# Performance work log

Hardware: AMD Instinct MI355X
Metric: run time of the kernel (lower is better)

Reference implementation:

```python
import jax, jax.numpy as jnp
import numpy as np


def _rms_norm(x, g, eps=1e-6):
    # WanRMSNorm over the full channel dim
    return x * jax.lax.rsqrt(jnp.mean(x * x, axis=-1, keepdims=True) + eps) * g


def _rope_apply(x, angles, f, h, w, start_frame):
    # x: [B, L, n, d]; angles: [1024, d//2] (real rotation angles; torch version
    # stores exp(i*theta) complex and multiplies in float64 -- same rotation math).
    B, L, n, d = x.shape
    c = d // 2
    c1 = c // 3
    c0 = c - 2 * c1  # band split [22, 21, 21] for c=64
    af = angles[start_frame:start_frame + f, :c0]        # [f, c0]
    ah = angles[:h, c0:c0 + c1]                          # [h, c1]
    aw = angles[:w, c0 + c1:]                            # [w, c1]
    ang = jnp.concatenate([
        jnp.broadcast_to(af[:, None, None, :], (f, h, w, c0)),
        jnp.broadcast_to(ah[None, :, None, :], (f, h, w, c1)),
        jnp.broadcast_to(aw[None, None, :, :], (f, h, w, c1)),
    ], axis=-1).reshape(1, L, 1, c)
    cos, sin = jnp.cos(ang), jnp.sin(ang)
    xr = x.reshape(B, L, n, c, 2)
    re, im = xr[..., 0], xr[..., 1]  # consecutive-pair complex layout
    out = jnp.stack([re * cos - im * sin, re * sin + im * cos], axis=-1)
    return out.reshape(B, L, n, d)


def reference(x, freqs, Wq, bq, Wk, bk, Wv, bv, Wo, bo, gq, gk,
              f, h, w, num_heads, local_attn_size, sink_size, start_frame):
    B, L, dim = x.shape
    n = num_heads
    d = dim // n
    # QKV projections + RMSNorm on q,k over full dim (as in the module)
    q = _rms_norm(x @ Wq.T + bq, gq).reshape(B, L, n, d)
    k = _rms_norm(x @ Wk.T + bk, gk).reshape(B, L, n, d)
    v = (x @ Wv.T + bv).reshape(B, L, n, d)
    rq = _rope_apply(q, freqs, f, h, w, start_frame)
    rk = _rope_apply(k, freqs, f, h, w, start_frame)
    # frame-level causal + local window + sink mask (the flex_attention block_mask)
    frame_idx = jnp.arange(L) // (h * w)
    fi, fj = frame_idx[:, None], frame_idx[None, :]
    mask = (fj <= fi) & ((fi - fj < local_attn_size) | (fj < sink_size))  # [L, L]
    scores = jnp.einsum('bqhd,bkhd->bhqk', rq, rk) / np.float32(np.sqrt(d))
    scores = jnp.where(mask, scores, -jnp.inf)
    p = jax.nn.softmax(scores, axis=-1)
    out = jnp.einsum('bhqk,bkhd->bqhd', p, v).reshape(B, L, dim)
    return out @ Wo.T + bo


def setup_inputs() -> dict:
    key = jax.random.key(0)
    dim, num_heads = 1536, 12
    f, h, w = 3, 30, 52
    L = f * h * w  # 4680
    d = dim // num_heads  # 128
    c = d // 2  # 64
    ks = jax.random.split(key, 6)
    scale = 0.02
    def lin(k):
        return jax.random.normal(k, (dim, dim), jnp.float32) * scale
    x = jax.random.normal(ks[0], (1, L, dim), jnp.float32)
    inv = 1.0 / (10000.0 ** (np.arange(c, dtype=np.float64) / c))
    freqs = jnp.asarray(np.outer(np.arange(1024), inv), jnp.float32)
    return {
        'x': x, 'freqs': freqs,
        'Wq': lin(ks[1]), 'bq': jnp.zeros(dim, jnp.float32),
        'Wk': lin(ks[2]), 'bk': jnp.zeros(dim, jnp.float32),
        'Wv': lin(ks[3]), 'bv': jnp.zeros(dim, jnp.float32),
        'Wo': lin(ks[4]), 'bo': jnp.zeros(dim, jnp.float32),
        'gq': jnp.ones(dim, jnp.float32), 'gk': jnp.ones(dim, jnp.float32),
        'f': f, 'h': h, 'w': w, 'num_heads': num_heads,
        'local_attn_size': 3, 'sink_size': 1, 'start_frame': 0,
    }
```

## Files before the change

### kernel.cpp

```cpp
#include <hip/hip_runtime.h>
#include <hip/hip_bf16.h>
#include <math.h>

typedef __bf16 bf16_t;
typedef __attribute__((ext_vector_type(8))) __bf16 bf16x8;
typedef __attribute__((ext_vector_type(4))) __bf16 bf16x4;
typedef __attribute__((ext_vector_type(4))) float f32x4;
typedef __attribute__((ext_vector_type(4))) short s16x4;

#define L_TOK 4680
#define DIM   1536
#define NH    12
#define HD    128
#define FRAME 1560
#define LPAD  4736
#define SCALE 0.08838834764831845f

union PU { bf16x4 h; s16x4 s; };

static __device__ __forceinline__ f32x4 mfma16(const PU& a, const PU& b, f32x4 c) {
#if defined(__HIP_DEVICE_COMPILE__)
  return __builtin_amdgcn_mfma_f32_16x16x16bf16_1k(a.s, b.s, c, 0, 0, 0);
#else
  (void)a; (void)b;
  return c;
#endif
}

__device__ __forceinline__ void gl_lds16(const bf16_t* g, bf16_t* l) {
  __builtin_amdgcn_global_load_lds(
      (const __attribute__((address_space(1))) unsigned int*)(g),
      (__attribute__((address_space(3))) unsigned int*)(l),
      16, 0, 0);
}

__global__ __launch_bounds__(256) void cast_f32_bf16(const float* __restrict__ in,
                                                     bf16_t* __restrict__ out, int n4) {
  int i = blockIdx.x * 256 + threadIdx.x;
  if (i >= n4) return;
  float4 v = ((const float4*)in)[i];
  bf16x4 o;
  o[0] = (__bf16)v.x; o[1] = (__bf16)v.y; o[2] = (__bf16)v.z; o[3] = (__bf16)v.w;
  ((bf16x4*)out)[i] = o;
}

__global__ __launch_bounds__(256) void gemm_qkv(
    const bf16_t* __restrict__ X,
    const bf16_t* __restrict__ Wq, const bf16_t* __restrict__ Wk, const bf16_t* __restrict__ Wv,
    const float* __restrict__ bq, const float* __restrict__ bk, const float* __restrict__ bv,
    bf16_t* __restrict__ Qo, bf16_t* __restrict__ Ko, bf16_t* __restrict__ Vt)
{
  __shared__ __align__(16) bf16_t Al[128 * 32];
  __shared__ __align__(16) bf16_t Bl[128 * 32];
  const int m0 = blockIdx.x * 128;
  const int nb = blockIdx.y;
  const int seg = nb / 12;
  const int n0 = (nb % 12) * 128;
  const bf16_t* W   = (seg == 0) ? Wq : (seg == 1) ? Wk : Wv;
  const float* bias = (seg == 0) ? bq : (seg == 1) ? bk : bv;

  const int tid = threadIdx.x;
  const int wave = tid >> 6, lane = tid & 63;
  const int quad = lane >> 4, l15 = lane & 15;
  const int wm = (wave >> 1) * 64, wn = (wave & 1) * 64;

  f32x4 acc[4][4];
#pragma unroll
  for (int i = 0; i < 4; ++i)
#pragma unroll
    for (int j = 0; j < 4; ++j) acc[i][j] = (f32x4){0.f, 0.f, 0.f, 0.f};

  const int c0 = wave * 2;
  const int fi0 = c0 * 512 + lane * 8;
  const int r0 = fi0 >> 5, col0 = fi0 & 31;
  const int fi1 = fi0 + 512;
  const int r1 = fi1 >> 5, col1 = fi1 & 31;

  const bf16_t* agp0 = X + (size_t)(m0 + r0) * DIM + col0;
  const bf16_t* agp1 = X + (size_t)(m0 + r1) * DIM + col1;
  const bf16_t* bgp0 = W + (size_t)(n0 + r0) * DIM + col0;
  const bf16_t* bgp1 = W + (size_t)(n0 + r1) * DIM + col1;
  bf16_t* al0 = Al + c0 * 512 + lane * 8;
  bf16_t* al1 = al0 + 512;
  bf16_t* bl0 = Bl + c0 * 512 + lane * 8;
  bf16_t* bl1 = bl0 + 512;

  for (int k0 = 0; k0 < DIM; k0 += 32) {
    __syncthreads();
    gl_lds16(agp0 + k0, al0);
    gl_lds16(agp1 + k0, al1);
    gl_lds16(bgp0 + k0, bl0);
    gl_lds16(bgp1 + k0, bl1);
    __syncthreads();
    bf16x8 af[4], bfg[4];
#pragma unroll
    for (int i = 0; i < 4; ++i) {
      af[i]  = *(const bf16x8*)(Al + (wm + i * 16 + l15) * 32 + quad * 8);
      bfg[i] = *(const bf16x8*)(Bl + (wn + i * 16 + l15) * 32 + quad * 8);
    }
#pragma unroll
    for (int i = 0; i < 4; ++i)
#pragma unroll
      for (int j = 0; j < 4; ++j)
        acc[i][j] = __builtin_amdgcn_mfma_f32_16x16x32_bf16(af[i], bfg[j], acc[i][j], 0, 0, 0);
  }

  if (seg < 2) {
    bf16_t* Out = (seg == 0) ? Qo : Ko;
#pragma unroll
    for (int i = 0; i < 4; ++i) {
#pragma unroll
      for (int j = 0; j < 4; ++j) {
        const int n = n0 + wn + j * 16 + l15;
        const float bb = bias[n];
#pragma unroll
        for (int r = 0; r < 4; ++r) {
          const int m = m0 + wm + i * 16 + quad * 4 + r;
          if (m < L_TOK) Out[(size_t)m * DIM + n] = (bf16_t)(acc[i][j][r] + bb);
        }
      }
    }
  } else {
#pragma unroll
    for (int i = 0; i < 4; ++i) {
      const int mb = m0 + wm + i * 16 + quad * 4;
      if (mb < L_TOK) {
#pragma unroll
        for (int j = 0; j < 4; ++j) {
          const int n = n0 + wn + j * 16 + l15;
          const float bb = bias[n];
          bf16x4 p;
          p[0] = (__bf16)(acc[i][j][0] + bb);
          p[1] = (__bf16)(acc[i][j][1] + bb);
          p[2] = (__bf16)(acc[i][j][2] + bb);
          p[3] = (__bf16)(acc[i][j][3] + bb);
          *(bf16x4*)(Vt + (size_t)n * LPAD + mb) = p;
        }
      }
    }
  }
}

__global__ __launch_bounds__(256) void rmsnorm_rope(
    bf16_t* __restrict__ Q, bf16_t* __restrict__ K,
    const float* __restrict__ gq, const float* __restrict__ gk,
    const float* __restrict__ freqs)
{
  const int l = blockIdx.x;
  const int tid = threadIdx.x;
  const int wave = tid >> 6, lane = tid & 63;
  bf16_t* qrow = Q + (size_t)l * DIM;
  bf16_t* krow = K + (size_t)l * DIM;

  unsigned int qb[3], kb[3];
  float sq = 0.f, sk = 0.f;
#pragma unroll
  for (int s = 0; s < 3; ++s) {
    const int p = s * 256 + tid;
    qb[s] = *(const unsigned int*)(qrow + 2 * p);
    kb[s] = *(const unsigned int*)(krow + 2 * p);
    const __bf16* qh = (const __bf16*)&qb[s];
    const __bf16* kh = (const __bf16*)&kb[s];
    const float q0 = (float)qh[0], q1 = (float)qh[1];
    const float k0 = (float)kh[0], k1 = (float)kh[1];
    sq += q0 * q0 + q1 * q1;
    sk += k0 * k0 + k1 * k1;
  }
#pragma unroll
  for (int off = 1; off < 64; off <<= 1) {
    sq += __shfl_xor(sq, off);
    sk += __shfl_xor(sk, off);
  }
  __shared__ float rq_s[4], rk_s[4];
  if (lane == 0) { rq_s[wave] = sq; rk_s[wave] = sk; }
  __syncthreads();
  sq = rq_s[0] + rq_s[1] + rq_s[2] + rq_s[3];
  sk = rk_s[0] + rk_s[1] + rk_s[2] + rk_s[3];
  const float rnq = rsqrtf(sq * (1.f / DIM) + 1e-6f);
  const float rnk = rsqrtf(sk * (1.f / DIM) + 1e-6f);

  const int t = l / FRAME;
  const int rem = l - t * FRAME;
  const int hh = rem / 52;
  const int ww = rem - hh * 52;

#pragma unroll
  for (int s = 0; s < 3; ++s) {
    const int p = s * 256 + tid;
    const int j = p & 63;
    const int sel = (j < 22) ? t : (j < 43) ? hh : ww;
    const float ang = freqs[sel * 64 + j];
    float sn, cs;
    __sincosf(ang, &sn, &cs);
    const __bf16* qh = (const __bf16*)&qb[s];
    const __bf16* kh = (const __bf16*)&kb[s];
    {
      const float g0 = gq[2 * p], g1 = gq[2 * p + 1];
      const float re = (float)qh[0] * rnq * g0;
      const float im = (float)qh[1] * rnq * g1;
      unsigned int o;
      __bf16* oh = (__bf16*)&o;
      oh[0] = (__bf16)((re * cs - im * sn) * SCALE);
      oh[1] = (__bf16)((re * sn + im * cs) * SCALE);
      *(unsigned int*)(qrow + 2 * p) = o;
    }
    {
      const float g0 = gk[2 * p], g1 = gk[2 * p + 1];
      const float re = (float)kh[0] * rnk * g0;
      const float im = (float)kh[1] * rnk * g1;
      unsigned int o;
      __bf16* oh = (__bf16*)&o;
      oh[0] = (__bf16)(re * cs - im * sn);
      oh[1] = (__bf16)(re * sn + im * cs);
      *(unsigned int*)(krow + 2 * p) = o;
    }
  }
}

template <bool SPLIT2>
__global__ __launch_bounds__(256) void attn(
    const bf16_t* __restrict__ Q, const bf16_t* __restrict__ K,
    const bf16_t* __restrict__ Vt, bf16_t* __restrict__ O,
    float* __restrict__ Opart, float* __restrict__ Mp, float* __restrict__ Lp)
{
  __shared__ __align__(16) bf16_t Kl[64 * 128];
  __shared__ __align__(16) bf16_t Vl[128 * 64];

  const int qb = (int)gridDim.x - 1 - (int)blockIdx.x;
  const int h  = blockIdx.y;
  const int slice = SPLIT2 ? blockIdx.z : 0;
  const int NS = SPLIT2 ? 2 : 1;
  const int tid = threadIdx.x;
  const int wave = tid >> 6, lane = tid & 63;
  const int quad = lane >> 4, l15 = lane & 15;
  const int e7 = l15 & 7, qh2 = quad >> 1, ql1 = quad & 1;
  const int q0 = qb * 128;
  const int qw = q0 + wave * 32;

  bf16x8 qf[2][4];
#pragma unroll
  for (int qt = 0; qt < 2; ++qt) {
    const int qrow = qw + qt * 16 + l15;
    const bf16_t* qp = Q + (size_t)qrow * DIM + h * HD + quad * 8;
#pragma unroll
    for (int ds = 0; ds < 4; ++ds) qf[qt][ds] = *(const bf16x8*)(qp + ds * 32);
  }

  int kendq[2];
#pragma unroll
  for (int qt = 0; qt < 2; ++qt) {
    int row = qw + qt * 16 + l15;
    if (row > L_TOK - 1) row = L_TOK - 1;
    kendq[qt] = FRAME * (row / FRAME + 1);
  }
  const int kend_blk = FRAME * (q0 / FRAME + 1);

  float m_run[2] = {-3.0e38f, -3.0e38f};
  float l_run[2] = {0.f, 0.f};
  f32x4 oacc[2][8];
#pragma unroll
  for (int qt = 0; qt < 2; ++qt)
#pragma unroll
    for (int nt = 0; nt < 8; ++nt) oacc[qt][nt] = (f32x4){0.f, 0.f, 0.f, 0.f};

  int lastl = q0 + 127; if (lastl > L_TOK - 1) lastl = L_TOK - 1;
  const int nkt = (FRAME * (lastl / FRAME + 1) + 63) >> 6;

  for (int kt = slice; kt < nkt; kt += NS) {
    const int kb = kt * 64;
    __syncthreads();
    uint4 tk[2], tv[2];
#pragma unroll
    for (int it = 0; it < 2; ++it) {
      const int c = tid + it * 512;
      const int r = c >> 4, cc = c & 15;
      tk[it] = *(const uint4*)(K + (size_t)(kb + r) * DIM + h * HD + cc * 8);
      const int d = c >> 3, c8 = c & 7;
      tv[it] = *(const uint4*)(Vt + (size_t)(h * HD + d) * LPAD + kb + c8 * 8);
    }
    uint4 tk2[2], tv2[2];
#pragma unroll
    for (int it = 0; it < 2; ++it) {
      const int c = tid + 256 + it * 512;
      const int r = c >> 4, cc = c & 15;
      tk2[it] = *(const uint4*)(K + (size_t)(kb + r) * DIM + h * HD + cc * 8);
      const int d = c >> 3, c8 = c & 7;
      tv2[it] = *(const uint4*)(Vt + (size_t)(h * HD + d) * LPAD + kb + c8 * 8);
    }
#pragma unroll
    for (int it = 0; it < 2; ++it) {
      const int c = tid + it * 512;
      const int r = c >> 4, cc = c & 15;
      *(uint4*)(Kl + r * 128 + ((cc ^ (r & 7)) * 8)) = tk[it];
      const int d = c >> 3, c8 = c & 7;
      *(uint4*)(Vl + d * 64 + ((c8 ^ (d & 7)) * 8)) = tv[it];
    }
#pragma unroll
    for (int it = 0; it < 2; ++it) {
      const int c = tid + 256 + it * 512;
      const int r = c >> 4, cc = c & 15;
      *(uint4*)(Kl + r * 128 + ((cc ^ (r & 7)) * 8)) = tk2[it];
      const int d = c >> 3, c8 = c & 7;
      *(uint4*)(Vl + d * 64 + ((c8 ^ (d & 7)) * 8)) = tv2[it];
    }
    __syncthreads();

    f32x4 s[4][2];
#pragma unroll
    for (int t4 = 0; t4 < 4; ++t4)
#pragma unroll
      for (int qt = 0; qt < 2; ++qt) s[t4][qt] = (f32x4){0.f, 0.f, 0.f, 0.f};
#pragma unroll
    for (int ds = 0; ds < 4; ++ds) {
      bf16x8 kf[4];
#pragma unroll
      for (int t4 = 0; t4 < 4; ++t4)
        kf[t4] = *(const bf16x8*)(Kl + (t4 * 16 + l15) * 128 + (((ds * 4 + quad) ^ e7) * 8));
#pragma unroll
      for (int t4 = 0; t4 < 4; ++t4) {
        s[t4][0] = __builtin_amdgcn_mfma_f32_16x16x32_bf16(kf[t4], qf[0][ds], s[t4][0], 0, 0, 0);
        s[t4][1] = __builtin_amdgcn_mfma_f32_16x16x32_bf16(kf[t4], qf[1][ds], s[t4][1], 0, 0, 0);
      }
    }

    if (kb + 64 > kend_blk) {
#pragma unroll
      for (int t4 = 0; t4 < 4; ++t4)
#pragma unroll
        for (int qt = 0; qt < 2; ++qt)
#pragma unroll
          for (int r = 0; r < 4; ++r) {
            const int key = kb + t4 * 16 + quad * 4 + r;
            if (key >= kendq[qt]) s[t4][qt][r] = -3.0e38f;
          }
    }

    float alpha[2];
    int need = 0;
#pragma unroll
    for (int qt = 0; qt < 2; ++qt) {
      f32x4 m4;
#pragma unroll
      for (int r = 0; r < 4; ++r)
        m4[r] = fmaxf(fmaxf(s[0][qt][r], s[1][qt][r]), fmaxf(s[2][qt][r], s[3][qt][r]));
      float mx = fmaxf(fmaxf(m4[0], m4[1]), fmaxf(m4[2], m4[3]));
      mx = fmaxf(mx, __shfl_xor(mx, 16));
      mx = fmaxf(mx, __shfl_xor(mx, 32));
      const float m_new = fmaxf(m_run[qt], mx);
      alpha[qt] = __expf(m_run[qt] - m_new);
      m_run[qt] = m_new;
      need |= (alpha[qt] != 1.0f);
    }
    if (__any(need)) {
#pragma unroll
      for (int qt = 0; qt < 2; ++qt)
#pragma unroll
        for (int nt = 0; nt < 8; ++nt)
#pragma unroll
          for (int r = 0; r < 4; ++r) oacc[qt][nt][r] *= alpha[qt];
    }

    PU u[4][2];
#pragma unroll
    for (int qt = 0; qt < 2; ++qt) {
      f32x4 a4 = (f32x4){0.f, 0.f, 0.f, 0.f};
#pragma unroll
      for (int t4 = 0; t4 < 4; ++t4) {
#pragma unroll
        for (int r = 0; r < 4; ++r) {
          const float e = __expf(s[t4][qt][r] - m_run[qt]);
          u[t4][qt].h[r] = (bf16_t)e;
          a4[r] += e;
        }
      }
      float ssum = (a4[0] + a4[1]) + (a4[2] + a4[3]);
      ssum += __shfl_xor(ssum, 16);
      ssum += __shfl_xor(ssum, 32);
      l_run[qt] = l_run[qt] * alpha[qt] + ssum;
    }

#pragma unroll
    for (int t4 = 0; t4 < 4; ++t4) {
#pragma unroll
      for (int nt = 0; nt < 8; ++nt) {
        const int row = nt * 16 + l15;
        PU vf;
        vf.h = *(const bf16x4*)(Vl + row * 64 + (((t4 * 2 + qh2) ^ e7) * 8) + ql1 * 4);
        oacc[0][nt] = mfma16(vf, u[t4][0], oacc[0][nt]);
        oacc[1][nt] = mfma16(vf, u[t4][1], oacc[1][nt]);
      }
    }
  }

  if (!SPLIT2) {
#pragma unroll
    for (int qt = 0; qt < 2; ++qt) {
      const float inv = 1.0f / l_run[qt];
      const int q = qw + qt * 16 + l15;
#pragma unroll
      for (int nt = 0; nt < 8; ++nt) {
        bf16x4 o;
#pragma unroll
        for (int r = 0; r < 4; ++r) o[r] = (bf16_t)(oacc[qt][nt][r] * inv);
        *(bf16x4*)(O + (size_t)q * DIM + h * HD + nt * 16 + quad * 4) = o;
      }
    }
  } else {
#pragma unroll
    for (int qt = 0; qt < 2; ++qt) {
      const int q = qw + qt * 16 + l15;
      float* op = Opart + ((size_t)slice * LPAD + q) * DIM + h * HD;
#pragma unroll
      for (int nt = 0; nt < 8; ++nt)
        *(f32x4*)(op + nt * 16 + quad * 4) = oacc[qt][nt];
      if (quad == 0) {
        Mp[(slice * NH + h) * LPAD + q] = m_run[qt];
        Lp[(slice * NH + h) * LPAD + q] = l_run[qt];
      }
    }
  }
}

__global__ __launch_bounds__(256) void attn_merge(
    const float* __restrict__ Op, const float* __restrict__ Mp,
    const float* __restrict__ Lp, bf16_t* __restrict__ Ob)
{
  const int idx = blockIdx.x * 256 + threadIdx.x;
  const int q = idx / (DIM / 4);
  const int c4 = idx - q * (DIM / 4);
  const int h = c4 >> 5;
  const float m0 = Mp[h * LPAD + q];
  const float m1 = Mp[(NH + h) * LPAD + q];
  const float l0 = Lp[h * LPAD + q];
  const float l1 = Lp[(NH + h) * LPAD + q];
  const float M = fmaxf(m0, m1);
  float w0 = __expf(m0 - M), w1 = __expf(m1 - M);
  const float inv = 1.0f / (l0 * w0 + l1 * w1);
  w0 *= inv; w1 *= inv;
  const float4 o0 = ((const float4*)Op)[idx];
  const float4 o1 = ((const float4*)Op)[idx + (size_t)LPAD * DIM / 4];
  bf16x4 o;
  o[0] = (bf16_t)(o0.x * w0 + o1.x * w1);
  o[1] = (bf16_t)(o0.y * w0 + o1.y * w1);
  o[2] = (bf16_t)(o0.z * w0 + o1.z * w1);
  o[3] = (bf16_t)(o0.w * w0 + o1.w * w1);
  ((bf16x4*)Ob)[idx] = o;
}

__global__ __launch_bounds__(256) void gemm_proj(
    const bf16_t* __restrict__ A, const bf16_t* __restrict__ W,
    const float* __restrict__ bias, float* __restrict__ out)
{
  __shared__ __align__(16) bf16_t Al[128 * 32];
  __shared__ __align__(16) bf16_t Bl[128 * 32];
  const int m0 = blockIdx.x * 128;
  const int n0 = blockIdx.y * 128;

  const int tid = threadIdx.x;
  const int wave = tid >> 6, lane = tid & 63;
  const int quad = lane >> 4, l15 = lane & 15;
  const int wm = (wave >> 1) * 64, wn = (wave & 1) * 64;

  f32x4 acc[4][4];
#pragma unroll
  for (int i = 0; i < 4; ++i)
#pragma unroll
    for (int j = 0; j < 4; ++j) acc[i][j] = (f32x4){0.f, 0.f, 0.f, 0.f};

  const int c0 = wave * 2;
  const int fi0 = c0 * 512 + lane * 8;
  const int r0 = fi0 >> 5, col0 = fi0 & 31;
  const int fi1 = fi0 + 512;
  const int r1 = fi1 >> 5, col1 = fi1 & 31;

  const bf16_t* agp0 = A + (size_t)(m0 + r0) * DIM + col0;
  const bf16_t* agp1 = A + (size_t)(m0 + r1) * DIM + col1;
  const bf16_t* bgp0 = W + (size_t)(n0 + r0) * DIM + col0;
  const bf16_t* bgp1 = W + (size_t)(n0 + r1) * DIM + col1;
  bf16_t* al0 = Al + c0 * 512 + lane * 8;
  bf16_t* al1 = al0 + 512;
  bf16_t* bl0 = Bl + c0 * 512 + lane * 8;
  bf16_t* bl1 = bl0 + 512;

  for (int k0 = 0; k0 < DIM; k0 += 32) {
    __syncthreads();
    gl_lds16(agp0 + k0, al0);
    gl_lds16(agp1 + k0, al1);
    gl_lds16(bgp0 + k0, bl0);
    gl_lds16(bgp1 + k0, bl1);
    __syncthreads();
    bf16x8 af[4], bfg[4];
#pragma unroll
    for (int i = 0; i < 4; ++i) {
      af[i]  = *(const bf16x8*)(Al + (wm + i * 16 + l15) * 32 + quad * 8);
      bfg[i] = *(const bf16x8*)(Bl + (wn + i * 16 + l15) * 32 + quad * 8);
    }
#pragma unroll
    for (int i = 0; i < 4; ++i)
#pragma unroll
      for (int j = 0; j < 4; ++j)
        acc[i][j] = __builtin_amdgcn_mfma_f32_16x16x32_bf16(af[i], bfg[j], acc[i][j], 0, 0, 0);
  }

#pragma unroll
  for (int i = 0; i < 4; ++i) {
#pragma unroll
    for (int j = 0; j < 4; ++j) {
      const int n = n0 + wn + j * 16 + l15;
      const float bb = bias[n];
#pragma unroll
      for (int r = 0; r < 4; ++r) {
        const int m = m0 + wm + i * 16 + quad * 4 + r;
        if (m < L_TOK) out[(size_t)m * DIM + n] = acc[i][j][r] + bb;
      }
    }
  }
}

extern "C" void kernel_launch(void* const* d_in, const int* in_sizes, int n_in,
                              void* d_out, int out_size, void* d_ws, size_t ws_size,
                              hipStream_t stream) {
  (void)in_sizes; (void)n_in; (void)out_size;
  const float* x  = (const float*)d_in[0];
  const float* fr = (const float*)d_in[1];
  const float* Wq = (const float*)d_in[2];
  const float* bq = (const float*)d_in[3];
  const float* Wk = (const float*)d_in[4];
  const float* bk = (const float*)d_in[5];
  const float* Wv = (const float*)d_in[6];
  const float* bv = (const float*)d_in[7];
  const float* Wo = (const float*)d_in[8];
  const float* bo = (const float*)d_in[9];
  const float* gq = (const float*)d_in[10];
  const float* gk = (const float*)d_in[11];
  float* out = (float*)d_out;

  char* ws = (char*)d_ws;
  size_t off = 0;
  auto alloc = [&](size_t bytes) {
    char* p = ws + off;
    off += (bytes + 255) & ~(size_t)255;
    return p;
  };
  const size_t lbuf = (size_t)LPAD * DIM * 2;
  const size_t wbuf = (size_t)DIM * DIM * 2;
  bf16_t* xb  = (bf16_t*)alloc(lbuf);
  bf16_t* Wqb = (bf16_t*)alloc(wbuf);
  bf16_t* Wkb = (bf16_t*)alloc(wbuf);
  bf16_t* Wvb = (bf16_t*)alloc(wbuf);
  bf16_t* Wob = (bf16_t*)alloc(wbuf);
  bf16_t* Qb  = (bf16_t*)alloc(lbuf);
  bf16_t* Kb  = (bf16_t*)alloc(lbuf);
  bf16_t* Vtb = (bf16_t*)alloc(lbuf);
  bf16_t* Ob  = (bf16_t*)alloc(lbuf);
  const size_t base_off = off;
  float* Opart = (float*)alloc((size_t)2 * LPAD * DIM * 4);
  float* Mp    = (float*)alloc((size_t)2 * NH * LPAD * 4);
  float* Lp    = (float*)alloc((size_t)2 * NH * LPAD * 4);
  const bool use_split = (off <= ws_size);
  if (base_off > ws_size) return;

  const int n4x = L_TOK * DIM / 4;
  const int n4w = DIM * DIM / 4;
  cast_f32_bf16<<<(n4x + 255) / 256, 256, 0, stream>>>(x, xb, n4x);
  cast_f32_bf16<<<(n4w + 255) / 256, 256, 0, stream>>>(Wq, Wqb, n4w);
  cast_f32_bf16<<<(n4w + 255) / 256, 256, 0, stream>>>(Wk, Wkb, n4w);
  cast_f32_bf16<<<(n4w + 255) / 256, 256, 0, stream>>>(Wv, Wvb, n4w);
  cast_f32_bf16<<<(n4w + 255) / 256, 256, 0, stream>>>(Wo, Wob, n4w);

  gemm_qkv<<<dim3(LPAD / 128, 36), 256, 0, stream>>>(xb, Wqb, Wkb, Wvb, bq, bk, bv,
                                                     Qb, Kb, Vtb);
  rmsnorm_rope<<<L_TOK, 256, 0, stream>>>(Qb, Kb, gq, gk, fr);
  if (use_split) {
    attn<true><<<dim3(LPAD / 128, NH, 2), 256, 0, stream>>>(Qb, Kb, Vtb, Ob, Opart, Mp, Lp);
    attn_merge<<<(LPAD * DIM / 4) / 256, 256, 0, stream>>>(Opart, Mp, Lp, Ob);
  } else {
    attn<false><<<dim3(LPAD / 128, NH, 1), 256, 0, stream>>>(Qb, Kb, Vtb, Ob, Opart, Mp, Lp);
  }
  gemm_proj<<<dim3(LPAD / 128, 12), 256, 0, stream>>>(Ob, Wob, bo, out);
}
```

Baseline: 576.6 us.

## Balance attention split-KV by query block and prefetch K/V tiles

Replaces the uniform 2-way KV split with variable chunking: early query blocks get one chunk, later blocks two or three, so the grid of 75 blocks per head is balanced against the growing causal key range. Adds register prefetch of the next K/V tile during compute, and stores partial outputs as bf16 instead of fp32 so the merge kernel moves less data. The merge now handles up to three partials with 8-wide vector loads. Storing partials in bf16 gives up some precision, and the hard-coded chunk mapping assumes this exact sequence length.

```diff
diff --git a/kernel.cpp b/kernel.cpp
--- a/kernel.cpp
+++ b/kernel.cpp
@@ -217,19 +217,25 @@
   }
 }
 
-template <bool SPLIT2>
+template <bool CHUNKED>
 __global__ __launch_bounds__(256) void attn(
     const bf16_t* __restrict__ Q, const bf16_t* __restrict__ K,
     const bf16_t* __restrict__ Vt, bf16_t* __restrict__ O,
-    float* __restrict__ Opart, float* __restrict__ Mp, float* __restrict__ Lp)
+    bf16_t* __restrict__ Op, float* __restrict__ Mp, float* __restrict__ Lp)
 {
   __shared__ __align__(16) bf16_t Kl[64 * 128];
   __shared__ __align__(16) bf16_t Vl[128 * 64];
 
-  const int qb = (int)gridDim.x - 1 - (int)blockIdx.x;
+  int qb, nc, c0i;
+  if (CHUNKED) {
+    const int c = blockIdx.x;
+    if (c < 12)      { qb = c;                 nc = 1; c0i = 0; }
+    else if (c < 36) { qb = 12 + (c - 12) / 2; nc = 2; c0i = (c - 12) % 2; }
+    else             { qb = 24 + (c - 36) / 3; nc = 3; c0i = (c - 36) % 3; }
+  } else {
+    qb = (int)gridDim.x - 1 - (int)blockIdx.x; nc = 1; c0i = 0;
+  }
   const int h  = blockIdx.y;
-  const int slice = SPLIT2 ? blockIdx.z : 0;
-  const int NS = SPLIT2 ? 2 : 1;
   const int tid = threadIdx.x;
   const int wave = tid >> 6, lane = tid & 63;
   const int quad = lane >> 4, l15 = lane & 15;
@@ -266,44 +272,38 @@
   int lastl = q0 + 127; if (lastl > L_TOK - 1) lastl = L_TOK - 1;
   const int nkt = (FRAME * (lastl / FRAME + 1) + 63) >> 6;
 
-  for (int kt = slice; kt < nkt; kt += NS) {
+  const int kr = tid >> 4, kc = tid & 15;
+  const int vd = tid >> 3, vc = tid & 7;
+  uint4 tk[4], tv[4];
+
+  auto ldt = [&](int kt) {
+    const int kb = kt * 64;
+#pragma unroll
+    for (int it = 0; it < 4; ++it) {
+      const int r = kr + it * 16;
+      tk[it] = *(const uint4*)(K + (size_t)(kb + r) * DIM + h * HD + kc * 8);
+      const int d = vd + it * 32;
+      tv[it] = *(const uint4*)(Vt + (size_t)(h * HD + d) * LPAD + kb + vc * 8);
+    }
+  };
+
+  ldt(c0i);
+  for (int kt = c0i; kt < nkt; kt += nc) {
     const int kb = kt * 64;
     __syncthreads();
-    uint4 tk[2], tv[2];
-#pragma unroll
-    for (int it = 0; it < 2; ++it) {
-      const int c = tid + it * 512;
-      const int r = c >> 4, cc = c & 15;
-      tk[it] = *(const uint4*)(K + (size_t)(kb + r) * DIM + h * HD + cc * 8);
-      const int d = c >> 3, c8 = c & 7;
-      tv[it] = *(const uint4*)(Vt + (size_t)(h * HD + d) * LPAD + kb + c8 * 8);
-    }
-    uint4 tk2[2], tv2[2];
-#pragma unroll
-    for (int it = 0; it < 2; ++it) {
-      const int c = tid + 256 + it * 512;
-      const int r = c >> 4, cc = c & 15;
-      tk2[it] = *(const uint4*)(K + (size_t)(kb + r) * DIM + h * HD + cc * 8);
-      const int d = c >> 3, c8 = c & 7;
-      tv2[it] = *(const uint4*)(Vt + (size_t)(h * HD + d) * LPAD + kb + c8 * 8);
-    }
-#pragma unroll
-    for (int it = 0; it < 2; ++it) {
-      const int c = tid + it * 512;
-      const int r = c >> 4, cc = c & 15;
-      *(uint4*)(Kl + r * 128 + ((cc ^ (r & 7)) * 8)) = tk[it];
-      const int d = c >> 3, c8 = c & 7;
-      *(uint4*)(Vl + d * 64 + ((c8 ^ (d & 7)) * 8)) = tv[it];
-    }
-#pragma unroll
-    for (int it = 0; it < 2; ++it) {
-      const int c = tid + 256 + it * 512;
-      const int r = c >> 4, cc = c & 15;
-      *(uint4*)(Kl + r * 128 + ((cc ^ (r & 7)) * 8)) = tk2[it];
-      const int d = c >> 3, c8 = c & 7;
-      *(uint4*)(Vl + d * 64 + ((c8 ^ (d & 7)) * 8)) = tv2[it];
+#pragma unroll
+    for (int it = 0; it < 4; ++it) {
+      const int r = kr + it * 16;
+      *(uint4*)(Kl + r * 128 + ((kc ^ (r & 7)) * 8)) = tk[it];
+      const int d = vd + it * 32;
+      *(uint4*)(Vl + d * 64 + ((vc ^ (d & 7)) * 8)) = tv[it];
     }
     __syncthreads();
+    {
+      int ktn = kt + nc;
+      if (ktn >= nkt) ktn = kt;
+      ldt(ktn);
+    }
 
     f32x4 s[4][2];
 #pragma unroll
@@ -392,59 +392,66 @@
     }
   }
 
-  if (!SPLIT2) {
-#pragma unroll
-    for (int qt = 0; qt < 2; ++qt) {
-      const float inv = 1.0f / l_run[qt];
-      const int q = qw + qt * 16 + l15;
-#pragma unroll
-      for (int nt = 0; nt < 8; ++nt) {
-        bf16x4 o;
-#pragma unroll
-        for (int r = 0; r < 4; ++r) o[r] = (bf16_t)(oacc[qt][nt][r] * inv);
-        *(bf16x4*)(O + (size_t)q * DIM + h * HD + nt * 16 + quad * 4) = o;
-      }
-    }
-  } else {
-#pragma unroll
-    for (int qt = 0; qt < 2; ++qt) {
-      const int q = qw + qt * 16 + l15;
-      float* op = Opart + ((size_t)slice * LPAD + q) * DIM + h * HD;
-#pragma unroll
-      for (int nt = 0; nt < 8; ++nt)
-        *(f32x4*)(op + nt * 16 + quad * 4) = oacc[qt][nt];
-      if (quad == 0) {
-        Mp[(slice * NH + h) * LPAD + q] = m_run[qt];
-        Lp[(slice * NH + h) * LPAD + q] = l_run[qt];
-      }
+#pragma unroll
+  for (int qt = 0; qt < 2; ++qt) {
+    const float inv = 1.0f / l_run[qt];
+    const int q = qw + qt * 16 + l15;
+    bf16_t* op = CHUNKED ? (Op + ((size_t)c0i * LPAD + q) * DIM + h * HD)
+                         : (O + (size_t)q * DIM + h * HD);
+    if (!CHUNKED && q >= L_TOK) continue;
+#pragma unroll
+    for (int nt = 0; nt < 8; ++nt) {
+      bf16x4 o;
+#pragma unroll
+      for (int r = 0; r < 4; ++r) o[r] = (bf16_t)(oacc[qt][nt][r] * inv);
+      *(bf16x4*)(op + nt * 16 + quad * 4) = o;
+    }
+    if (CHUNKED && quad == 0) {
+      Mp[(c0i * NH + h) * LPAD + q] = m_run[qt];
+      Lp[(c0i * NH + h) * LPAD + q] = l_run[qt];
     }
   }
 }
 
 __global__ __launch_bounds__(256) void attn_merge(
-    const float* __restrict__ Op, const float* __restrict__ Mp,
+    const bf16_t* __restrict__ Op, const float* __restrict__ Mp,
     const float* __restrict__ Lp, bf16_t* __restrict__ Ob)
 {
   const int idx = blockIdx.x * 256 + threadIdx.x;
-  const int q = idx / (DIM / 4);
-  const int c4 = idx - q * (DIM / 4);
-  const int h = c4 >> 5;
-  const float m0 = Mp[h * LPAD + q];
-  const float m1 = Mp[(NH + h) * LPAD + q];
-  const float l0 = Lp[h * LPAD + q];
-  const float l1 = Lp[(NH + h) * LPAD + q];
-  const float M = fmaxf(m0, m1);
-  float w0 = __expf(m0 - M), w1 = __expf(m1 - M);
-  const float inv = 1.0f / (l0 * w0 + l1 * w1);
-  w0 *= inv; w1 *= inv;
-  const float4 o0 = ((const float4*)Op)[idx];
-  const float4 o1 = ((const float4*)Op)[idx + (size_t)LPAD * DIM / 4];
-  bf16x4 o;
-  o[0] = (bf16_t)(o0.x * w0 + o1.x * w1);
-  o[1] = (bf16_t)(o0.y * w0 + o1.y * w1);
-  o[2] = (bf16_t)(o0.z * w0 + o1.z * w1);
-  o[3] = (bf16_t)(o0.w * w0 + o1.w * w1);
-  ((bf16x4*)Ob)[idx] = o;
+  const int q = idx / (DIM / 8);
+  const int c8 = idx - q * (DIM / 8);
+  const int h = c8 / (HD / 8);
+  const int qb = ((q < L_TOK) ? q : (L_TOK - 1)) >> 7;
+  const int nc = (qb < 12) ? 1 : (qb < 24) ? 2 : 3;
+
+  float mv[3], lv[3];
+  float M = -3.0e38f;
+#pragma unroll
+  for (int s = 0; s < 3; ++s)
+    if (s < nc) {
+      mv[s] = Mp[(s * NH + h) * LPAD + q];
+      lv[s] = Lp[(s * NH + h) * LPAD + q];
+      M = fmaxf(M, mv[s]);
+    }
+  float w[3] = {0.f, 0.f, 0.f};
+  float den = 0.f;
+#pragma unroll
+  for (int s = 0; s < 3; ++s)
+    if (s < nc) { w[s] = __expf(mv[s] - M) * lv[s]; den += w[s]; }
+  const float inv = 1.0f / den;
+
+  float acc[8] = {0.f, 0.f, 0.f, 0.f, 0.f, 0.f, 0.f, 0.f};
+#pragma unroll
+  for (int s = 0; s < 3; ++s)
+    if (s < nc) {
+      bf16x8 o = *(const bf16x8*)(Op + ((size_t)s * LPAD + q) * DIM + c8 * 8);
+#pragma unroll
+      for (int j = 0; j < 8; ++j) acc[j] += (float)o[j] * w[s];
+    }
+  bf16x8 r;
+#pragma unroll
+  for (int j = 0; j < 8; ++j) r[j] = (bf16_t)(acc[j] * inv);
+  *(bf16x8*)(Ob + (size_t)q * DIM + c8 * 8) = r;
 }
 
 __global__ __launch_bounds__(256) void gemm_proj(
@@ -554,10 +561,10 @@
   bf16_t* Vtb = (bf16_t*)alloc(lbuf);
   bf16_t* Ob  = (bf16_t*)alloc(lbuf);
   const size_t base_off = off;
-  float* Opart = (float*)alloc((size_t)2 * LPAD * DIM * 4);
-  float* Mp    = (float*)alloc((size_t)2 * NH * LPAD * 4);
-  float* Lp    = (float*)alloc((size_t)2 * NH * LPAD * 4);
-  const bool use_split = (off <= ws_size);
+  bf16_t* Opc = (bf16_t*)alloc((size_t)3 * LPAD * DIM * 2);
+  float* Mp   = (float*)alloc((size_t)3 * NH * LPAD * 4);
+  float* Lp   = (float*)alloc((size_t)3 * NH * LPAD * 4);
+  const bool use_chunked = (off <= ws_size);
   if (base_off > ws_size) return;
 
   const int n4x = L_TOK * DIM / 4;
@@ -571,11 +578,11 @@
   gemm_qkv<<<dim3(LPAD / 128, 36), 256, 0, stream>>>(xb, Wqb, Wkb, Wvb, bq, bk, bv,
                                                      Qb, Kb, Vtb);
   rmsnorm_rope<<<L_TOK, 256, 0, stream>>>(Qb, Kb, gq, gk, fr);
-  if (use_split) {
-    attn<true><<<dim3(LPAD / 128, NH, 2), 256, 0, stream>>>(Qb, Kb, Vtb, Ob, Opart, Mp, Lp);
-    attn_merge<<<(LPAD * DIM / 4) / 256, 256, 0, stream>>>(Opart, Mp, Lp, Ob);
+  if (use_chunked) {
+    attn<true><<<dim3(75, NH), 256, 0, stream>>>(Qb, Kb, Vtb, Ob, Opc, Mp, Lp);
+    attn_merge<<<(LPAD * DIM / 8) / 256, 256, 0, stream>>>(Opc, Mp, Lp, Ob);
   } else {
-    attn<false><<<dim3(LPAD / 128, NH, 1), 256, 0, stream>>>(Qb, Kb, Vtb, Ob, Opart, Mp, Lp);
+    attn<false><<<dim3(LPAD / 128, NH), 256, 0, stream>>>(Qb, Kb, Vtb, Ob, Opc, Mp, Lp);
   }
   gemm_proj<<<dim3(LPAD / 128, 12), 256, 0, stream>>>(Ob, Wob, bo, out);
 }
```

Result: slower. 681.3 us (+18.1%).
